# Performance work log

Hardware: AMD Instinct MI355X
Metric: run time of the kernel (lower is better)

The kernel has to match this reference:

```python
import jax, jax.numpy as jnp
import numpy as np
import math

FREQS = jnp.array([1., 2., 4., 8., 7., 5.], dtype=jnp.float32)  # default frequencies


def setup_inputs() -> dict:
    key = jax.random.key(0)
    k1, k2, k3 = jax.random.split(key, 3)
    B, N, H, F = 8, 4096, 256, 6
    x = jax.random.normal(k1, (B, N, H), dtype=jnp.float32)
    t = jax.random.uniform(k2, (B, 1), dtype=jnp.float32) * (2.0 * math.pi)
    oscillators = jax.random.normal(k3, (F, H, H), dtype=jnp.float32) * 0.1
    # phase_shifts[i] = i / F * pi, broadcast over hidden dim (matches torch init)
    phase_shifts = jnp.broadcast_to(
        (jnp.arange(F, dtype=jnp.float32) / F * math.pi)[:, None], (F, H)
    ).copy()
    return {"x": x, "t": t, "oscillators": oscillators, "phase_shifts": phase_shifts}


def reference(x, t, oscillators, phase_shifts):
    # resonator[b, f, h] = sin(freq_f * t[b, 0] + phase[f, h])
    res = jnp.sin(FREQS[None, :, None] * t[:, :, None] + phase_shifts[None, :, :])  # [B, F, H]
    # result[b, n, k] = sum_f (x[b, n, :] @ W_f)[k] * res[b, f, k]
    return jnp.einsum('bnh,fhk,bfk->bnk', x, oscillators, res)
```

## Files before the change

### kernel.cpp

```cpp
#include <hip/hip_runtime.h>
#include <hip/hip_bf16.h>


#define B_  8
#define N_  4096
#define H_  256

typedef __attribute__((ext_vector_type(8))) short s8v;
typedef __attribute__((ext_vector_type(4))) float f4v;

#define LGK_BARRIER() asm volatile("s_waitcnt lgkmcnt(0)\n\ts_barrier" ::: "memory")

__global__ __launch_bounds__(256) void build_w(
    const float* __restrict__ osc,
    const float* __restrict__ t,
    const float* __restrict__ phase,
    __hip_bfloat16* __restrict__ Wt)
{
    const float freqs[6] = {1.f, 2.f, 4.f, 8.f, 7.f, 5.f};
    __shared__ float tr[16 * 68];

    const int b  = blockIdx.z;
    const int n0 = blockIdx.y * 64;
    const int h0 = blockIdx.x * 16;
    const int tid = threadIdx.x;

    const float tb = t[b];
    const int nr = (tid & 15) * 4;
    const int hr = tid >> 4;
    float s[6][4];
#pragma unroll
    for (int f = 0; f < 6; ++f)
#pragma unroll
        for (int j = 0; j < 4; ++j)
            s[f][j] = __sinf(freqs[f] * tb + phase[f * 256 + n0 + nr + j]);

    const int h = h0 + hr;
    float4 acc = make_float4(0.f, 0.f, 0.f, 0.f);
#pragma unroll
    for (int f = 0; f < 6; ++f) {
        float4 o = *(const float4*)&osc[f * 65536 + h * 256 + n0 + nr];
        acc.x += o.x * s[f][0];
        acc.y += o.y * s[f][1];
        acc.z += o.z * s[f][2];
        acc.w += o.w * s[f][3];
    }
    *(float4*)&tr[hr * 68 + nr] = acc;
    __syncthreads();

    const int nw = tid >> 2;
    const int hw = (tid & 3) * 4;
    float v0 = tr[(hw + 0) * 68 + nw];
    float v1 = tr[(hw + 1) * 68 + nw];
    float v2 = tr[(hw + 2) * 68 + nw];
    float v3 = tr[(hw + 3) * 68 + nw];
    union { __hip_bfloat162 h2[2]; unsigned long long q; } cv;
    cv.h2[0] = __float22bfloat162_rn(make_float2(v0, v1));
    cv.h2[1] = __float22bfloat162_rn(make_float2(v2, v3));
    *(unsigned long long*)(Wt + (size_t)b * 65536 + (size_t)(n0 + nw) * 256 + h0 + hw) = cv.q;
}

#define LDST 72

__global__ __launch_bounds__(512, 4) void gemm(
    const float* __restrict__ X,
    const __hip_bfloat16* __restrict__ Wt,
    float* __restrict__ out)
{
    __shared__ short As[64 * LDST];
    __shared__ short Bs[256 * LDST];

    const int b     = blockIdx.y;
    const int mTile = blockIdx.x;

    const int tid    = threadIdx.x;
    const int lane   = tid & 63;
    const int wave   = tid >> 6;
    const int lane15 = lane & 15;
    const int quad   = lane >> 4;
    const int wm     = wave >> 2;
    const int wn     = wave & 3;

    const float* Xb          = X   + (size_t)b * N_ * H_ + (size_t)mTile * 64 * H_;
    const __hip_bfloat16* Wb = Wt  + (size_t)b * H_ * H_;
    float* Ob                = out + (size_t)b * N_ * H_ + (size_t)mTile * 64 * H_;

    const int arow = tid >> 3;
    const int aseg = (tid & 7) * 8;
    const float* pa = Xb + (size_t)arow * H_ + aseg;

    const int brow = tid >> 1;
    const int bhf  = (tid & 1) * 32;
    const __hip_bfloat16* pb = Wb + (size_t)brow * H_ + bhf;

    f4v acc[2][4] = {};

    float4 a0[2], a1[2];
    uint4  bv[2][4];
#pragma unroll
    for (int sl = 0; sl < 2; ++sl) {
        const int k = sl * 64;
        a0[sl] = *(const float4*)(pa + k);
        a1[sl] = *(const float4*)(pa + k + 4);
#pragma unroll
        for (int j = 0; j < 4; ++j)
            bv[sl][j] = *(const uint4*)(pb + k + j * 8);
    }

    for (int it = 0; it < 4; ++it) {
        const int sl = it & 1;
        union { __hip_bfloat162 h2[4]; uint4 q; } cv;
        cv.h2[0] = __float22bfloat162_rn(make_float2(a0[sl].x, a0[sl].y));
        cv.h2[1] = __float22bfloat162_rn(make_float2(a0[sl].z, a0[sl].w));
        cv.h2[2] = __float22bfloat162_rn(make_float2(a1[sl].x, a1[sl].y));
        cv.h2[3] = __float22bfloat162_rn(make_float2(a1[sl].z, a1[sl].w));
        *(uint4*)(&As[arow * LDST + aseg]) = cv.q;
        *(uint4*)(&Bs[brow * LDST + bhf + 0])  = bv[sl][0];
        *(uint4*)(&Bs[brow * LDST + bhf + 8])  = bv[sl][1];
        *(uint4*)(&Bs[brow * LDST + bhf + 16]) = bv[sl][2];
        *(uint4*)(&Bs[brow * LDST + bhf + 24]) = bv[sl][3];
        LGK_BARRIER();

        if (it < 2) {
            const int k = (it + 2) * 64;
            a0[sl] = *(const float4*)(pa + k);
            a1[sl] = *(const float4*)(pa + k + 4);
#pragma unroll
            for (int j = 0; j < 4; ++j)
                bv[sl][j] = *(const uint4*)(pb + k + j * 8);
        }

#pragma unroll
        for (int kh = 0; kh < 2; ++kh) {
            s8v af[2], bf[4];
#pragma unroll
            for (int mt = 0; mt < 2; ++mt)
                af[mt] = *(const s8v*)(&As[(wm * 32 + mt * 16 + lane15) * LDST + kh * 32 + quad * 8]);
#pragma unroll
            for (int nt = 0; nt < 4; ++nt)
                bf[nt] = *(const s8v*)(&Bs[(wn * 64 + nt * 16 + lane15) * LDST + kh * 32 + quad * 8]);
#pragma unroll
            for (int mt = 0; mt < 2; ++mt)
#pragma unroll
                for (int nt = 0; nt < 4; ++nt)
                    acc[mt][nt] = __builtin_amdgcn_mfma_f32_16x16x32_bf16(
                        af[mt], bf[nt], acc[mt][nt], 0, 0, 0);
        }
        LGK_BARRIER();
    }

#pragma unroll
    for (int mt = 0; mt < 2; ++mt) {
#pragma unroll
        for (int r = 0; r < 4; ++r) {
            int row = wm * 32 + mt * 16 + quad * 4 + r;
            float* po = Ob + (size_t)row * H_ + wn * 64 + lane15;
#pragma unroll
            for (int nt = 0; nt < 4; ++nt)
                __builtin_nontemporal_store(acc[mt][nt][r], po + nt * 16);
        }
    }
}

extern "C" void kernel_launch(void* const* d_in, const int* in_sizes, int n_in,
                              void* d_out, int out_size, void* d_ws, size_t ws_size,
                              hipStream_t stream) {
    const float* x     = (const float*)d_in[0];
    const float* t     = (const float*)d_in[1];
    const float* osc   = (const float*)d_in[2];
    const float* phase = (const float*)d_in[3];
    __hip_bfloat16* Wt = (__hip_bfloat16*)d_ws;
    float* out = (float*)d_out;

    dim3 gw(16, 4, 8);
    build_w<<<gw, 256, 0, stream>>>(osc, t, phase, Wt);

    dim3 gg(64, 8);
    gemm<<<gg, 512, 0, stream>>>(x, Wt, out);
}
```

Before: 93.76 us.

## Fuse weight construction into GEMM kernel with per-block shared-memory W

```diff
diff --git a/kernel.cpp b/kernel.cpp
--- a/kernel.cpp
+++ b/kernel.cpp
@@ -11,69 +11,83 @@
 
 #define LGK_BARRIER() asm volatile("s_waitcnt lgkmcnt(0)\n\ts_barrier" ::: "memory")
 
-__global__ __launch_bounds__(256) void build_w(
+#define LDW 264
+#define LDA 72
+
+__device__ __constant__ float c_freqs[6] = {1.f, 2.f, 4.f, 8.f, 7.f, 5.f};
+
+__global__ __launch_bounds__(512, 2) void fused(
+    const float* __restrict__ X,
+    const float* __restrict__ t,
     const float* __restrict__ osc,
-    const float* __restrict__ t,
     const float* __restrict__ phase,
-    __hip_bfloat16* __restrict__ Wt)
-{
-    const float freqs[6] = {1.f, 2.f, 4.f, 8.f, 7.f, 5.f};
-    __shared__ float tr[16 * 68];
-
-    const int b  = blockIdx.z;
-    const int n0 = blockIdx.y * 64;
-    const int h0 = blockIdx.x * 16;
-    const int tid = threadIdx.x;
-
-    const float tb = t[b];
-    const int nr = (tid & 15) * 4;
-    const int hr = tid >> 4;
-    float s[6][4];
-#pragma unroll
-    for (int f = 0; f < 6; ++f)
-#pragma unroll
-        for (int j = 0; j < 4; ++j)
-            s[f][j] = __sinf(freqs[f] * tb + phase[f * 256 + n0 + nr + j]);
-
-    const int h = h0 + hr;
-    float4 acc = make_float4(0.f, 0.f, 0.f, 0.f);
-#pragma unroll
-    for (int f = 0; f < 6; ++f) {
-        float4 o = *(const float4*)&osc[f * 65536 + h * 256 + n0 + nr];
-        acc.x += o.x * s[f][0];
-        acc.y += o.y * s[f][1];
-        acc.z += o.z * s[f][2];
-        acc.w += o.w * s[f][3];
-    }
-    *(float4*)&tr[hr * 68 + nr] = acc;
-    __syncthreads();
-
-    const int nw = tid >> 2;
-    const int hw = (tid & 3) * 4;
-    float v0 = tr[(hw + 0) * 68 + nw];
-    float v1 = tr[(hw + 1) * 68 + nw];
-    float v2 = tr[(hw + 2) * 68 + nw];
-    float v3 = tr[(hw + 3) * 68 + nw];
-    union { __hip_bfloat162 h2[2]; unsigned long long q; } cv;
-    cv.h2[0] = __float22bfloat162_rn(make_float2(v0, v1));
-    cv.h2[1] = __float22bfloat162_rn(make_float2(v2, v3));
-    *(unsigned long long*)(Wt + (size_t)b * 65536 + (size_t)(n0 + nw) * 256 + h0 + hw) = cv.q;
-}
-
-#define LDST 72
-
-__global__ __launch_bounds__(512, 4) void gemm(
-    const float* __restrict__ X,
-    const __hip_bfloat16* __restrict__ Wt,
     float* __restrict__ out)
 {
-    __shared__ short As[64 * LDST];
-    __shared__ short Bs[256 * LDST];
+    __shared__ short Wt[256 * LDW];
+    __shared__ union {
+        struct {
+            float s[6 * 256];
+            float tr[2][2][16 * 68];
+        } bld;
+        short As[128 * LDA];
+    } u;
 
     const int b     = blockIdx.y;
     const int mTile = blockIdx.x;
+    const int tid   = threadIdx.x;
 
-    const int tid    = threadIdx.x;
+    const float* Xb = X   + (size_t)b * N_ * H_ + (size_t)mTile * 128 * H_;
+    float* Ob       = out + (size_t)b * N_ * H_ + (size_t)mTile * 128 * H_;
+
+    const int arow = tid >> 2;
+    const int aseg = (tid & 3) * 16;
+    const float* pa = Xb + (size_t)arow * H_ + aseg;
+    float4 av[4][4];
+#pragma unroll
+    for (int sl = 0; sl < 4; ++sl)
+#pragma unroll
+        for (int j = 0; j < 4; ++j)
+            av[sl][j] = *(const float4*)(pa + sl * 64 + j * 4);
+
+    const float tb = t[b];
+#pragma unroll
+    for (int k = 0; k < 3; ++k) {
+        int idx = tid + k * 512;
+        u.bld.s[idx] = __sinf(c_freqs[idx >> 8] * tb + phase[idx]);
+    }
+    LGK_BARRIER();
+
+    const int g  = tid >> 8;
+    const int tt = tid & 255;
+    const int nr = (tt & 15) * 4;
+    const int hr = tt >> 4;
+    const int nw = tt >> 2;
+    const int hw = (tt & 3) * 4;
+    for (int p = 0; p < 32; ++p) {
+        const int s  = p * 2 + g;
+        const int h0 = (s & 15) * 16;
+        const int n0 = (s >> 4) * 64;
+        float4 acc = make_float4(0.f, 0.f, 0.f, 0.f);
+#pragma unroll
+        for (int f = 0; f < 6; ++f) {
+            float4 sv = *(const float4*)&u.bld.s[f * 256 + n0 + nr];
+            float4 o  = *(const float4*)&osc[f * 65536 + (h0 + hr) * 256 + n0 + nr];
+            acc.x += o.x * sv.x;  acc.y += o.y * sv.y;
+            acc.z += o.z * sv.z;  acc.w += o.w * sv.w;
+        }
+        *(float4*)&u.bld.tr[g][p & 1][hr * 68 + nr] = acc;
+        LGK_BARRIER();
+        float v0 = u.bld.tr[g][p & 1][(hw + 0) * 68 + nw];
+        float v1 = u.bld.tr[g][p & 1][(hw + 1) * 68 + nw];
+        float v2 = u.bld.tr[g][p & 1][(hw + 2) * 68 + nw];
+        float v3 = u.bld.tr[g][p & 1][(hw + 3) * 68 + nw];
+        union { __hip_bfloat162 h2[2]; unsigned long long q; } cv;
+        cv.h2[0] = __float22bfloat162_rn(make_float2(v0, v1));
+        cv.h2[1] = __float22bfloat162_rn(make_float2(v2, v3));
+        *(unsigned long long*)&Wt[(n0 + nw) * LDW + h0 + hw] = cv.q;
+    }
+    LGK_BARRIER();
+
     const int lane   = tid & 63;
     const int wave   = tid >> 6;
     const int lane15 = lane & 15;
@@ -81,66 +95,34 @@
     const int wm     = wave >> 2;
     const int wn     = wave & 3;
 
-    const float* Xb          = X   + (size_t)b * N_ * H_ + (size_t)mTile * 64 * H_;
-    const __hip_bfloat16* Wb = Wt  + (size_t)b * H_ * H_;
-    float* Ob                = out + (size_t)b * N_ * H_ + (size_t)mTile * 64 * H_;
+    f4v acc[4][4] = {};
 
-    const int arow = tid >> 3;
-    const int aseg = (tid & 7) * 8;
-    const float* pa = Xb + (size_t)arow * H_ + aseg;
-
-    const int brow = tid >> 1;
-    const int bhf  = (tid & 1) * 32;
-    const __hip_bfloat16* pb = Wb + (size_t)brow * H_ + bhf;
-
-    f4v acc[2][4] = {};
-
-    float4 a0[2], a1[2];
-    uint4  bv[2][4];
 #pragma unroll
-    for (int sl = 0; sl < 2; ++sl) {
-        const int k = sl * 64;
-        a0[sl] = *(const float4*)(pa + k);
-        a1[sl] = *(const float4*)(pa + k + 4);
-#pragma unroll
-        for (int j = 0; j < 4; ++j)
-            bv[sl][j] = *(const uint4*)(pb + k + j * 8);
-    }
-
     for (int it = 0; it < 4; ++it) {
-        const int sl = it & 1;
-        union { __hip_bfloat162 h2[4]; uint4 q; } cv;
-        cv.h2[0] = __float22bfloat162_rn(make_float2(a0[sl].x, a0[sl].y));
-        cv.h2[1] = __float22bfloat162_rn(make_float2(a0[sl].z, a0[sl].w));
-        cv.h2[2] = __float22bfloat162_rn(make_float2(a1[sl].x, a1[sl].y));
-        cv.h2[3] = __float22bfloat162_rn(make_float2(a1[sl].z, a1[sl].w));
-        *(uint4*)(&As[arow * LDST + aseg]) = cv.q;
-        *(uint4*)(&Bs[brow * LDST + bhf + 0])  = bv[sl][0];
-        *(uint4*)(&Bs[brow * LDST + bhf + 8])  = bv[sl][1];
-        *(uint4*)(&Bs[brow * LDST + bhf + 16]) = bv[sl][2];
-        *(uint4*)(&Bs[brow * LDST + bhf + 24]) = bv[sl][3];
+        union { __hip_bfloat162 h2[4]; uint4 q; } c0, c1;
+        c0.h2[0] = __float22bfloat162_rn(make_float2(av[it][0].x, av[it][0].y));
+        c0.h2[1] = __float22bfloat162_rn(make_float2(av[it][0].z, av[it][0].w));
+        c0.h2[2] = __float22bfloat162_rn(make_float2(av[it][1].x, av[it][1].y));
+        c0.h2[3] = __float22bfloat162_rn(make_float2(av[it][1].z, av[it][1].w));
+        c1.h2[0] = __float22bfloat162_rn(make_float2(av[it][2].x, av[it][2].y));
+        c1.h2[1] = __float22bfloat162_rn(make_float2(av[it][2].z, av[it][2].w));
+        c1.h2[2] = __float22bfloat162_rn(make_float2(av[it][3].x, av[it][3].y));
+        c1.h2[3] = __float22bfloat162_rn(make_float2(av[it][3].z, av[it][3].w));
+        *(uint4*)&u.As[arow * LDA + aseg + 0] = c0.q;
+        *(uint4*)&u.As[arow * LDA + aseg + 8] = c1.q;
         LGK_BARRIER();
-
-        if (it < 2) {
-            const int k = (it + 2) * 64;
-            a0[sl] = *(const float4*)(pa + k);
-            a1[sl] = *(const float4*)(pa + k + 4);
-#pragma unroll
-            for (int j = 0; j < 4; ++j)
-                bv[sl][j] = *(const uint4*)(pb + k + j * 8);
-        }
 
 #pragma unroll
         for (int kh = 0; kh < 2; ++kh) {
-            s8v af[2], bf[4];
+            s8v af[4], bf[4];
 #pragma unroll
-            for (int mt = 0; mt < 2; ++mt)
-                af[mt] = *(const s8v*)(&As[(wm * 32 + mt * 16 + lane15) * LDST + kh * 32 + quad * 8]);
+            for (int mt = 0; mt < 4; ++mt)
+                af[mt] = *(const s8v*)&u.As[(wm * 64 + mt * 16 + lane15) * LDA + kh * 32 + quad * 8];
 #pragma unroll
             for (int nt = 0; nt < 4; ++nt)
-                bf[nt] = *(const s8v*)(&Bs[(wn * 64 + nt * 16 + lane15) * LDST + kh * 32 + quad * 8]);
+                bf[nt] = *(const s8v*)&Wt[(wn * 64 + nt * 16 + lane15) * LDW + it * 64 + kh * 32 + quad * 8];
 #pragma unroll
-            for (int mt = 0; mt < 2; ++mt)
+            for (int mt = 0; mt < 4; ++mt)
 #pragma unroll
                 for (int nt = 0; nt < 4; ++nt)
                     acc[mt][nt] = __builtin_amdgcn_mfma_f32_16x16x32_bf16(
@@ -150,10 +132,10 @@
     }
 
 #pragma unroll
-    for (int mt = 0; mt < 2; ++mt) {
+    for (int mt = 0; mt < 4; ++mt) {
 #pragma unroll
         for (int r = 0; r < 4; ++r) {
-            int row = wm * 32 + mt * 16 + quad * 4 + r;
+            int row = wm * 64 + mt * 16 + quad * 4 + r;
             float* po = Ob + (size_t)row * H_ + wn * 64 + lane15;
 #pragma unroll
             for (int nt = 0; nt < 4; ++nt)
@@ -169,12 +151,9 @@
     const float* t     = (const float*)d_in[1];
     const float* osc   = (const float*)d_in[2];
     const float* phase = (const float*)d_in[3];
-    __hip_bfloat16* Wt = (__hip_bfloat16*)d_ws;
-    float* out = (float*)d_out;
+    (void)d_ws; (void)ws_size;
+    (void)in_sizes; (void)n_in; (void)out_size;
 
-    dim3 gw(16, 4, 8);
-    build_w<<<gw, 256, 0, stream>>>(osc, t, phase, Wt);
-
-    dim3 gg(64, 8);
-    gemm<<<gg, 512, 0, stream>>>(x, Wt, out);
+    dim3 gg(32, 8);
+    fused<<<gg, 512, 0, stream>>>(x, t, osc, phase, (float*)d_out);
 }
```

After: 123.2 us. +31.4%, slower.

## Load GEMM operands directly into MFMA fragments, dropping LDS staging

Applied to the files above, without the earlier changes.

```diff
diff --git a/kernel.cpp b/kernel.cpp
--- a/kernel.cpp
+++ b/kernel.cpp
@@ -8,8 +8,6 @@
 
 typedef __attribute__((ext_vector_type(8))) short s8v;
 typedef __attribute__((ext_vector_type(4))) float f4v;
-
-#define LGK_BARRIER() asm volatile("s_waitcnt lgkmcnt(0)\n\ts_barrier" ::: "memory")
 
 __global__ __launch_bounds__(256) void build_w(
     const float* __restrict__ osc,
@@ -60,16 +58,11 @@
     *(unsigned long long*)(Wt + (size_t)b * 65536 + (size_t)(n0 + nw) * 256 + h0 + hw) = cv.q;
 }
 
-#define LDST 72
-
 __global__ __launch_bounds__(512, 4) void gemm(
     const float* __restrict__ X,
     const __hip_bfloat16* __restrict__ Wt,
     float* __restrict__ out)
 {
-    __shared__ short As[64 * LDST];
-    __shared__ short Bs[256 * LDST];
-
     const int b     = blockIdx.y;
     const int mTile = blockIdx.x;
 
@@ -85,68 +78,68 @@
     const __hip_bfloat16* Wb = Wt  + (size_t)b * H_ * H_;
     float* Ob                = out + (size_t)b * N_ * H_ + (size_t)mTile * 64 * H_;
 
-    const int arow = tid >> 3;
-    const int aseg = (tid & 7) * 8;
-    const float* pa = Xb + (size_t)arow * H_ + aseg;
-
-    const int brow = tid >> 1;
-    const int bhf  = (tid & 1) * 32;
-    const __hip_bfloat16* pb = Wb + (size_t)brow * H_ + bhf;
+    const float* pa[2];
+#pragma unroll
+    for (int mt = 0; mt < 2; ++mt)
+        pa[mt] = Xb + (size_t)(wm * 32 + mt * 16 + lane15) * H_ + quad * 8;
+    const __hip_bfloat16* pb[4];
+#pragma unroll
+    for (int nt = 0; nt < 4; ++nt)
+        pb[nt] = Wb + (size_t)(wn * 64 + nt * 16 + lane15) * H_ + quad * 8;
 
     f4v acc[2][4] = {};
 
-    float4 a0[2], a1[2];
-    uint4  bv[2][4];
+    float4 av[2][2][2];
+    s8v    bv[2][4];
 #pragma unroll
     for (int sl = 0; sl < 2; ++sl) {
-        const int k = sl * 64;
-        a0[sl] = *(const float4*)(pa + k);
-        a1[sl] = *(const float4*)(pa + k + 4);
+        const int k = sl * 32;
 #pragma unroll
-        for (int j = 0; j < 4; ++j)
-            bv[sl][j] = *(const uint4*)(pb + k + j * 8);
+        for (int mt = 0; mt < 2; ++mt) {
+            av[sl][mt][0] = *(const float4*)(pa[mt] + k);
+            av[sl][mt][1] = *(const float4*)(pa[mt] + k + 4);
+        }
+#pragma unroll
+        for (int nt = 0; nt < 4; ++nt)
+            bv[sl][nt] = *(const s8v*)(pb[nt] + k);
     }
 
-    for (int it = 0; it < 4; ++it) {
-        const int sl = it & 1;
-        union { __hip_bfloat162 h2[4]; uint4 q; } cv;
-        cv.h2[0] = __float22bfloat162_rn(make_float2(a0[sl].x, a0[sl].y));
-        cv.h2[1] = __float22bfloat162_rn(make_float2(a0[sl].z, a0[sl].w));
-        cv.h2[2] = __float22bfloat162_rn(make_float2(a1[sl].x, a1[sl].y));
-        cv.h2[3] = __float22bfloat162_rn(make_float2(a1[sl].z, a1[sl].w));
-        *(uint4*)(&As[arow * LDST + aseg]) = cv.q;
-        *(uint4*)(&Bs[brow * LDST + bhf + 0])  = bv[sl][0];
-        *(uint4*)(&Bs[brow * LDST + bhf + 8])  = bv[sl][1];
-        *(uint4*)(&Bs[brow * LDST + bhf + 16]) = bv[sl][2];
-        *(uint4*)(&Bs[brow * LDST + bhf + 24]) = bv[sl][3];
-        LGK_BARRIER();
+#pragma unroll
+    for (int ks = 0; ks < 8; ++ks) {
+        const int sl = ks & 1;
 
-        if (it < 2) {
-            const int k = (it + 2) * 64;
-            a0[sl] = *(const float4*)(pa + k);
-            a1[sl] = *(const float4*)(pa + k + 4);
+        s8v af[2], bf[4];
 #pragma unroll
-            for (int j = 0; j < 4; ++j)
-                bv[sl][j] = *(const uint4*)(pb + k + j * 8);
+        for (int mt = 0; mt < 2; ++mt) {
+            union { __hip_bfloat162 h2[4]; s8v v; } cv;
+            cv.h2[0] = __float22bfloat162_rn(make_float2(av[sl][mt][0].x, av[sl][mt][0].y));
+            cv.h2[1] = __float22bfloat162_rn(make_float2(av[sl][mt][0].z, av[sl][mt][0].w));
+            cv.h2[2] = __float22bfloat162_rn(make_float2(av[sl][mt][1].x, av[sl][mt][1].y));
+            cv.h2[3] = __float22bfloat162_rn(make_float2(av[sl][mt][1].z, av[sl][mt][1].w));
+            af[mt] = cv.v;
+        }
+#pragma unroll
+        for (int nt = 0; nt < 4; ++nt)
+            bf[nt] = bv[sl][nt];
+
+        if (ks < 6) {
+            const int k = (ks + 2) * 32;
+#pragma unroll
+            for (int mt = 0; mt < 2; ++mt) {
+                av[sl][mt][0] = *(const float4*)(pa[mt] + k);
+                av[sl][mt][1] = *(const float4*)(pa[mt] + k + 4);
+            }
+#pragma unroll
+            for (int nt = 0; nt < 4; ++nt)
+                bv[sl][nt] = *(const s8v*)(pb[nt] + k);
         }
 
 #pragma unroll
-        for (int kh = 0; kh < 2; ++kh) {
-            s8v af[2], bf[4];
-#pragma unroll
-            for (int mt = 0; mt < 2; ++mt)
-                af[mt] = *(const s8v*)(&As[(wm * 32 + mt * 16 + lane15) * LDST + kh * 32 + quad * 8]);
+        for (int mt = 0; mt < 2; ++mt)
 #pragma unroll
             for (int nt = 0; nt < 4; ++nt)
-                bf[nt] = *(const s8v*)(&Bs[(wn * 64 + nt * 16 + lane15) * LDST + kh * 32 + quad * 8]);
-#pragma unroll
-            for (int mt = 0; mt < 2; ++mt)
-#pragma unroll
-                for (int nt = 0; nt < 4; ++nt)
-                    acc[mt][nt] = __builtin_amdgcn_mfma_f32_16x16x32_bf16(
-                        af[mt], bf[nt], acc[mt][nt], 0, 0, 0);
-        }
-        LGK_BARRIER();
+                acc[mt][nt] = __builtin_amdgcn_mfma_f32_16x16x32_bf16(
+                    af[mt], bf[nt], acc[mt][nt], 0, 0, 0);
     }
 
 #pragma unroll
@@ -171,6 +164,7 @@
     const float* phase = (const float*)d_in[3];
     __hip_bfloat16* Wt = (__hip_bfloat16*)d_ws;
     float* out = (float*)d_out;
+    (void)in_sizes; (void)n_in; (void)out_size; (void)ws_size;
 
     dim3 gw(16, 4, 8);
     build_w<<<gw, 256, 0, stream>>>(osc, t, phase, Wt);
```

Result: slower. 111.2 us (+18.6%).

## Load W tile directly into double-buffered LDS via global_load_lds with XOR swizzle

Applied to the files above, without the earlier changes.

```diff
diff --git a/kernel.cpp b/kernel.cpp
--- a/kernel.cpp
+++ b/kernel.cpp
@@ -9,7 +9,10 @@
 typedef __attribute__((ext_vector_type(8))) short s8v;
 typedef __attribute__((ext_vector_type(4))) float f4v;
 
-#define LGK_BARRIER() asm volatile("s_waitcnt lgkmcnt(0)\n\ts_barrier" ::: "memory")
+#define AS1 __attribute__((address_space(1)))
+#define AS3 __attribute__((address_space(3)))
+#define GLOAD_LDS16(g, l) \
+    __builtin_amdgcn_global_load_lds((const AS1 void*)(g), (AS3 void*)(l), 16, 0, 0)
 
 __global__ __launch_bounds__(256) void build_w(
     const float* __restrict__ osc,
@@ -60,15 +63,15 @@
     *(unsigned long long*)(Wt + (size_t)b * 65536 + (size_t)(n0 + nw) * 256 + h0 + hw) = cv.q;
 }
 
-#define LDST 72
+#define LDA 72
 
 __global__ __launch_bounds__(512, 4) void gemm(
     const float* __restrict__ X,
     const __hip_bfloat16* __restrict__ Wt,
     float* __restrict__ out)
 {
-    __shared__ short As[64 * LDST];
-    __shared__ short Bs[256 * LDST];
+    __shared__ short As[64 * LDA];
+    __shared__ short Bs[2][256 * 64];
 
     const int b     = blockIdx.y;
     const int mTile = blockIdx.x;
@@ -89,45 +92,39 @@
     const int aseg = (tid & 7) * 8;
     const float* pa = Xb + (size_t)arow * H_ + aseg;
 
-    const int brow = tid >> 1;
-    const int bhf  = (tid & 1) * 32;
-    const __hip_bfloat16* pb = Wb + (size_t)brow * H_ + bhf;
+    const int brow = lane >> 3;
+    const int bchk = (lane & 7) ^ brow;
+    const __hip_bfloat16* pbg = Wb + (size_t)(wave * 32 + brow) * H_ + bchk * 8;
 
     f4v acc[2][4] = {};
 
-    float4 a0[2], a1[2];
-    uint4  bv[2][4];
 #pragma unroll
-    for (int sl = 0; sl < 2; ++sl) {
-        const int k = sl * 64;
-        a0[sl] = *(const float4*)(pa + k);
-        a1[sl] = *(const float4*)(pa + k + 4);
+    for (int j = 0; j < 4; ++j)
+        GLOAD_LDS16(pbg + (size_t)j * 8 * H_, &Bs[0][wave * 2048 + j * 512]);
+    float4 av[2][2];
+    av[0][0] = *(const float4*)(pa + 0);
+    av[0][1] = *(const float4*)(pa + 4);
+
 #pragma unroll
-        for (int j = 0; j < 4; ++j)
-            bv[sl][j] = *(const uint4*)(pb + k + j * 8);
-    }
+    for (int it = 0; it < 4; ++it) {
+        const int p = it & 1;
+        union { __hip_bfloat162 h2[4]; uint4 q; } cv;
+        cv.h2[0] = __float22bfloat162_rn(make_float2(av[p][0].x, av[p][0].y));
+        cv.h2[1] = __float22bfloat162_rn(make_float2(av[p][0].z, av[p][0].w));
+        cv.h2[2] = __float22bfloat162_rn(make_float2(av[p][1].x, av[p][1].y));
+        cv.h2[3] = __float22bfloat162_rn(make_float2(av[p][1].z, av[p][1].w));
+        *(uint4*)&As[arow * LDA + aseg] = cv.q;
 
-    for (int it = 0; it < 4; ++it) {
-        const int sl = it & 1;
-        union { __hip_bfloat162 h2[4]; uint4 q; } cv;
-        cv.h2[0] = __float22bfloat162_rn(make_float2(a0[sl].x, a0[sl].y));
-        cv.h2[1] = __float22bfloat162_rn(make_float2(a0[sl].z, a0[sl].w));
-        cv.h2[2] = __float22bfloat162_rn(make_float2(a1[sl].x, a1[sl].y));
-        cv.h2[3] = __float22bfloat162_rn(make_float2(a1[sl].z, a1[sl].w));
-        *(uint4*)(&As[arow * LDST + aseg]) = cv.q;
-        *(uint4*)(&Bs[brow * LDST + bhf + 0])  = bv[sl][0];
-        *(uint4*)(&Bs[brow * LDST + bhf + 8])  = bv[sl][1];
-        *(uint4*)(&Bs[brow * LDST + bhf + 16]) = bv[sl][2];
-        *(uint4*)(&Bs[brow * LDST + bhf + 24]) = bv[sl][3];
-        LGK_BARRIER();
-
-        if (it < 2) {
-            const int k = (it + 2) * 64;
-            a0[sl] = *(const float4*)(pa + k);
-            a1[sl] = *(const float4*)(pa + k + 4);
+        if (it < 3) {
 #pragma unroll
             for (int j = 0; j < 4; ++j)
-                bv[sl][j] = *(const uint4*)(pb + k + j * 8);
+                GLOAD_LDS16(pbg + (it + 1) * 64 + (size_t)j * 8 * H_,
+                            &Bs[p ^ 1][wave * 2048 + j * 512]);
+            av[p ^ 1][0] = *(const float4*)(pa + (it + 1) * 64);
+            av[p ^ 1][1] = *(const float4*)(pa + (it + 1) * 64 + 4);
+            asm volatile("s_waitcnt vmcnt(6) lgkmcnt(0)\n\ts_barrier" ::: "memory");
+        } else {
+            asm volatile("s_waitcnt vmcnt(0) lgkmcnt(0)\n\ts_barrier" ::: "memory");
         }
 
 #pragma unroll
@@ -135,10 +132,13 @@
             s8v af[2], bf[4];
 #pragma unroll
             for (int mt = 0; mt < 2; ++mt)
-                af[mt] = *(const s8v*)(&As[(wm * 32 + mt * 16 + lane15) * LDST + kh * 32 + quad * 8]);
+                af[mt] = *(const s8v*)&As[(wm * 32 + mt * 16 + lane15) * LDA + kh * 32 + quad * 8];
 #pragma unroll
-            for (int nt = 0; nt < 4; ++nt)
-                bf[nt] = *(const s8v*)(&Bs[(wn * 64 + nt * 16 + lane15) * LDST + kh * 32 + quad * 8]);
+            for (int nt = 0; nt < 4; ++nt) {
+                const int n  = wn * 64 + nt * 16 + lane15;
+                const int pc = ((kh * 4 + quad) ^ (lane15 & 7)) * 8;
+                bf[nt] = *(const s8v*)&Bs[p][n * 64 + pc];
+            }
 #pragma unroll
             for (int mt = 0; mt < 2; ++mt)
 #pragma unroll
@@ -146,7 +146,8 @@
                     acc[mt][nt] = __builtin_amdgcn_mfma_f32_16x16x32_bf16(
                         af[mt], bf[nt], acc[mt][nt], 0, 0, 0);
         }
-        LGK_BARRIER();
+        if (it < 3)
+            asm volatile("s_barrier" ::: "memory");
     }
 
 #pragma unroll
@@ -171,6 +172,7 @@
     const float* phase = (const float*)d_in[3];
     __hip_bfloat16* Wt = (__hip_bfloat16*)d_ws;
     float* out = (float*)d_out;
+    (void)in_sizes; (void)n_in; (void)out_size; (void)ws_size;
 
     dim3 gw(16, 4, 8);
     build_w<<<gw, 256, 0, stream>>>(osc, t, phase, Wt);
```

Result: no change. 92.29 us (-1.6%).
